# Kernel optimization log

Hardware: AMD Instinct MI355X
Metric: run time of the kernel (lower is better)

The kernel has to match this reference:

```python
import jax, jax.numpy as jnp
import numpy as np

DIM = 512
NUM_HEADS = 8
HEAD_DIM = DIM // NUM_HEADS
SCALE = HEAD_DIM ** -0.5


def setup_inputs() -> dict:
    key = jax.random.key(0)
    k1, k2, k3, k4 = jax.random.split(key, 4)
    x = jax.random.normal(k1, (4, 2048, DIM), dtype=jnp.float32)
    W_qkv = jax.random.normal(k2, (DIM, 3 * DIM), dtype=jnp.float32) * (DIM ** -0.5)
    W_proj = jax.random.normal(k3, (DIM, DIM), dtype=jnp.float32) * (DIM ** -0.5)
    b_proj = jax.random.normal(k4, (DIM,), dtype=jnp.float32) * 0.01
    return {"x": x, "W_qkv": W_qkv, "W_proj": W_proj, "b_proj": b_proj}


def reference(x, W_qkv, W_proj, b_proj):
    B, N, C = x.shape
    H, hd = NUM_HEADS, HEAD_DIM
    # qkv: [B, N, 3, H, hd] -> (q, k, v) each [B, H, N, hd]
    qkv = (x @ W_qkv).reshape(B, N, 3, H, hd)
    qkv = jnp.transpose(qkv, (2, 0, 3, 1, 4))
    q, k, v = qkv[0], qkv[1], qkv[2]
    # eager attention: [B, H, N, N]
    attn = jnp.einsum('bhnd,bhmd->bhnm', q, k) * SCALE
    attn = jax.nn.softmax(attn, axis=-1)
    out = jnp.einsum('bhnm,bhmd->bhnd', attn, v)  # [B, H, N, hd]
    out = jnp.transpose(out, (0, 2, 1, 3)).reshape(B, N, C)
    out = out @ W_proj + b_proj
    return (out, k, v)
```

## Files before the change

kernel.cpp:

```cpp
#include <hip/hip_runtime.h>

typedef unsigned short ushort_t;
typedef __bf16 bf16x8 __attribute__((ext_vector_type(8)));
typedef ushort_t u16x8 __attribute__((ext_vector_type(8)));
typedef float f32x4 __attribute__((ext_vector_type(4)));

#define MFMA(a, b, c) __builtin_amdgcn_mfma_f32_16x16x32_bf16(a, b, c, 0, 0, 0)

#define N_X      4194304L
#define N_WQKV   786432L
#define N_WPROJ  262144L
#define OUT_OFF_K 4194304L
#define OUT_OFF_V 8388608L

#define OFF_FLAG   0UL
#define OFF_XB     1024UL
#define OFF_WQKVT  (OFF_XB + 8388608UL)
#define OFF_WPROJT (OFF_WQKVT + 1572864UL)
#define OFF_BPROJ  (OFF_WPROJT + 524288UL)
#define OFF_QB     (OFF_BPROJ + 2048UL)
#define OFF_KB     (OFF_QB + 8388608UL)
#define OFF_VTB    (OFF_KB + 8388608UL)
#define OFF_ATTN   (OFF_VTB + 8388608UL)

#define QSCALE 0.180336880519191f

__device__ __forceinline__ ushort_t f2b(float f) {
    union { float f; unsigned u; } v; v.f = f;
    return (ushort_t)((v.u + 0x7FFFu + ((v.u >> 16) & 1u)) >> 16);
}
__device__ __forceinline__ float b2f(ushort_t h) {
    union { unsigned u; float f; } v; v.u = ((unsigned)h) << 16;
    return v.f;
}

__device__ __forceinline__ float fast_exp2(float x) {
#if __has_builtin(__builtin_amdgcn_exp2f)
    return __builtin_amdgcn_exp2f(x);
#else
    return __expf(x * 0.6931471805599453f);
#endif
}

__device__ __forceinline__ void glds16(const void* g, const void* l) {
    __builtin_amdgcn_global_load_lds((__attribute__((address_space(1))) void*)g,
                                     (__attribute__((address_space(3))) void*)l,
                                     16, 0, 0);
}

__device__ __forceinline__ int detect_bf16(const unsigned* __restrict__ x) {
    int lane = threadIdx.x & 63;
    int cnt = 0;
#pragma unroll
    for (int i = 0; i < 4; ++i) {
        unsigned w = x[lane + i * 64];
        float v = __uint_as_float((w & 0xFFFFu) << 16);
        float a = fabsf(v);
        if (a > 1e-3f && a < 100.0f) cnt++;
    }
#pragma unroll
    for (int off = 1; off < 64; off <<= 1) cnt += __shfl_xor(cnt, off, 64);
    return cnt > 128;
}

__global__ void k_prep(const void* __restrict__ xv, const void* __restrict__ wqv,
                       const void* __restrict__ wpv, const void* __restrict__ bpv,
                       ushort_t* __restrict__ xb, ushort_t* __restrict__ wqT,
                       ushort_t* __restrict__ wpT, float* __restrict__ bpf) {
    const int isb = detect_bf16((const unsigned*)xv);
    long i0 = (long)blockIdx.x * blockDim.x + threadIdx.x;
    long stride = (long)gridDim.x * blockDim.x;
    if (isb) {
        const ushort_t* x = (const ushort_t*)xv;
        const ushort_t* wq = (const ushort_t*)wqv;
        const ushort_t* wp = (const ushort_t*)wpv;
        const ushort_t* bp = (const ushort_t*)bpv;
        for (long i = i0; i < N_X / 8; i += stride)
            ((u16x8*)xb)[i] = ((const u16x8*)x)[i];
        for (long i = i0; i < N_WQKV / 8; i += stride) {
            long n = (i * 8) >> 9, k = (i * 8) & 511;
            u16x8 o;
#pragma unroll
            for (int e = 0; e < 8; ++e) o[e] = wq[(k + e) * 1536 + n];
            ((u16x8*)wqT)[i] = o;
        }
        for (long i = i0; i < N_WPROJ / 8; i += stride) {
            long n = (i * 8) >> 9, k = (i * 8) & 511;
            u16x8 o;
#pragma unroll
            for (int e = 0; e < 8; ++e) o[e] = wp[(k + e) * 512 + n];
            ((u16x8*)wpT)[i] = o;
        }
        for (long i = i0; i < 512; i += stride) bpf[i] = b2f(bp[i]);
    } else {
        const float* x = (const float*)xv;
        const float* wq = (const float*)wqv;
        const float* wp = (const float*)wpv;
        const float* bp = (const float*)bpv;
        for (long i = i0; i < N_X / 8; i += stride) {
            f32x4 a = ((const f32x4*)x)[i * 2], b = ((const f32x4*)x)[i * 2 + 1];
            u16x8 o;
#pragma unroll
            for (int e = 0; e < 4; ++e) { o[e] = f2b(a[e]); o[e + 4] = f2b(b[e]); }
            ((u16x8*)xb)[i] = o;
        }
        for (long i = i0; i < N_WQKV / 8; i += stride) {
            long n = (i * 8) >> 9, k = (i * 8) & 511;
            u16x8 o;
#pragma unroll
            for (int e = 0; e < 8; ++e) o[e] = f2b(wq[(k + e) * 1536 + n]);
            ((u16x8*)wqT)[i] = o;
        }
        for (long i = i0; i < N_WPROJ / 8; i += stride) {
            long n = (i * 8) >> 9, k = (i * 8) & 511;
            u16x8 o;
#pragma unroll
            for (int e = 0; e < 8; ++e) o[e] = f2b(wp[(k + e) * 512 + n]);
            ((u16x8*)wpT)[i] = o;
        }
        for (long i = i0; i < 512; i += stride) bpf[i] = bp[i];
    }
}

__global__ __launch_bounds__(256, 2)
void k_qkv(const unsigned* __restrict__ xraw,
           const ushort_t* __restrict__ xb, const ushort_t* __restrict__ wqT,
           ushort_t* __restrict__ qb, ushort_t* __restrict__ kb, ushort_t* __restrict__ vb,
           void* __restrict__ dout) {
    const int isb = detect_bf16(xraw);
    __shared__ __align__(16) ushort_t As[128 * 32];
    __shared__ __align__(16) ushort_t Bs[128 * 32];
    const int tid = threadIdx.x, wave = tid >> 6, lane = tid & 63;
    const int id = blockIdx.x;
    const int xcd = id & 7, g = id >> 3;
    const int bx = xcd * 8 + (g & 7);
    const int by = g >> 3;
    const int tm = bx * 128, tn = by * 128;
    const int wm = (wave >> 1) * 64, wn = (wave & 1) * 64;
    const int l15 = lane & 15, lq = lane >> 4;
    const int srow = lane >> 2, sc = lane & 3;

    f32x4 acc[4][4];
#pragma unroll
    for (int a = 0; a < 4; ++a)
#pragma unroll
        for (int b = 0; b < 4; ++b) acc[a][b] = (f32x4){0.f, 0.f, 0.f, 0.f};

    for (int k0 = 0; k0 < 512; k0 += 32) {
#pragma unroll
        for (int t = 0; t < 2; ++t) {
            int s = wave * 2 + t;
            int row = s * 16 + srow;
            int c = (sc ^ (row >> 1)) & 3;
            glds16(xb  + (long)(tm + row) * 512 + k0 + c * 8, As + s * 512);
            glds16(wqT + (long)(tn + row) * 512 + k0 + c * 8, Bs + s * 512);
        }
        __syncthreads();
        bf16x8 af[4], bfr[4];
#pragma unroll
        for (int mt = 0; mt < 4; ++mt) {
            int row = wm + mt * 16 + l15;
            int cp = (lq ^ (row >> 1)) & 3;
            af[mt] = *(const bf16x8*)(As + row * 32 + cp * 8);
        }
#pragma unroll
        for (int nt = 0; nt < 4; ++nt) {
            int row = wn + nt * 16 + l15;
            int cp = (lq ^ (row >> 1)) & 3;
            bfr[nt] = *(const bf16x8*)(Bs + row * 32 + cp * 8);
        }
#pragma unroll
        for (int mt = 0; mt < 4; ++mt)
#pragma unroll
            for (int nt = 0; nt < 4; ++nt)
                acc[mt][nt] = MFMA(af[mt], bfr[nt], acc[mt][nt]);
        __syncthreads();
    }

    float*    koutf = (float*)dout + OUT_OFF_K;
    float*    voutf = (float*)dout + OUT_OFF_V;
    ushort_t* koutb = (ushort_t*)dout + OUT_OFF_K;
    ushort_t* voutb = (ushort_t*)dout + OUT_OFF_V;
#pragma unroll
    for (int mt = 0; mt < 4; ++mt) {
#pragma unroll
        for (int nt = 0; nt < 4; ++nt) {
            int j = tn + wn + nt * 16 + l15;
            int t = j >> 9, h = (j >> 6) & 7, d = j & 63;
#pragma unroll
            for (int r = 0; r < 4; ++r) {
                int mm = tm + wm + mt * 16 + lq * 4 + r;
                int b = mm >> 11, nn = mm & 2047;
                float v = acc[mt][nt][r];
                long idx = ((long)(b * 8 + h) * 2048 + nn) * 64 + d;
                if (t == 0) {
                    qb[idx] = f2b(v * QSCALE);
                } else if (t == 1) {
                    kb[idx] = f2b(v);
                    if (isb) koutb[idx] = f2b(v); else koutf[idx] = v;
                } else {
                    vb[idx] = f2b(v);
                    if (isb) voutb[idx] = f2b(v); else voutf[idx] = v;
                }
            }
        }
    }
}

__global__ __launch_bounds__(256, 4)
void k_vtrans(const ushort_t* __restrict__ vb, ushort_t* __restrict__ vtb) {
    __shared__ ushort_t T[64 * 64];
    const int tid = threadIdx.x;
    const int bh = blockIdx.y, ktile = blockIdx.x;
    const long base = (long)bh * 131072 + (long)ktile * 64 * 64;
    const int row = tid >> 2, cq = tid & 3;
#pragma unroll
    for (int half = 0; half < 2; ++half) {
        int c = cq + half * 4;
        u16x8 v = *(const u16x8*)(vb + base + row * 64 + c * 8);
#pragma unroll
        for (int e = 0; e < 8; ++e) {
            int dim = c * 8 + e;
            T[row * 64 + ((dim + row) & 63)] = v[e];
        }
    }
    __syncthreads();
#pragma unroll
    for (int it = 0; it < 16; ++it) {
        int d = (tid >> 6) * 16 + it;
        int key = tid & 63;
        vtb[(long)bh * 131072 + (long)d * 2048 + ktile * 64 + key] =
            T[key * 64 + ((d + key) & 63)];
    }
}

__global__ __launch_bounds__(256, 2)
void k_attn(const ushort_t* __restrict__ qb, const ushort_t* __restrict__ kb,
            const ushort_t* __restrict__ vtb, ushort_t* __restrict__ attnb) {
    __shared__ __align__(16) ushort_t Kt[2][128 * 64];
    __shared__ __align__(16) ushort_t Vt[2][64 * 128];
    const int tid = threadIdx.x, wave = tid >> 6, lane = tid & 63;
    const int l15 = lane & 15, lq = lane >> 4;
    const int id = blockIdx.x;
    const int xcd = id & 7, g = id >> 3;
    const int bh = xcd * 4 + (g >> 4);
    const int qt = g & 15;
    const long kvbase = (long)bh * 131072;
    const long qbase = kvbase + (long)qt * 128 * 64;

    const int ksrow = lane >> 3, kschunk = lane & 7;
    const int vsrow = lane >> 4, vschunk = lane & 15;

    auto stage = [&](int j, int buf) {
#pragma unroll
        for (int t = 0; t < 4; ++t) {
            int s = wave * 4 + t;
            {
                int p = s * 8 + ksrow;
                int pos = p & 15;
                int akey = ((p >> 5) << 5) + ((pos >> 2) << 3) + (pos & 3) + ((p >> 4) & 1) * 4;
                int c = kschunk ^ (p & 7);
                glds16(kb + kvbase + (long)(j * 128 + akey) * 64 + c * 8, &Kt[buf][s * 512]);
            }
            {
                int row = s * 4 + vsrow;
                int c = vschunk ^ (row & 15);
                glds16(vtb + kvbase + (long)row * 2048 + j * 128 + c * 8, &Vt[buf][s * 512]);
            }
        }
    };

    stage(0, 0);

    bf16x8 aQ[2][2];
#pragma unroll
    for (int mq = 0; mq < 2; ++mq)
#pragma unroll
        for (int kt = 0; kt < 2; ++kt)
            aQ[mq][kt] = *(const bf16x8*)(qb + qbase +
                (long)(wave * 32 + mq * 16 + l15) * 64 + kt * 32 + lq * 8);

    union { ushort_t u[8]; bf16x8 v; } oneu;
#pragma unroll
    for (int i = 0; i < 8; ++i) oneu.u[i] = 0x3F80;
    const bf16x8 ones8 = oneu.v;

    f32x4 oacc[2][4], sum_acc[2];
#pragma unroll
    for (int mq = 0; mq < 2; ++mq) {
#pragma unroll
        for (int nd = 0; nd < 4; ++nd) oacc[mq][nd] = (f32x4){0.f, 0.f, 0.f, 0.f};
        sum_acc[mq] = (f32x4){0.f, 0.f, 0.f, 0.f};
    }

    for (int j = 0; j < 16; ++j) {
        int cur = j & 1;
        if (j < 15) {
            stage(j + 1, cur ^ 1);
            asm volatile("s_waitcnt vmcnt(8)" ::: "memory");
        } else {
            asm volatile("s_waitcnt vmcnt(0)" ::: "memory");
        }
        __builtin_amdgcn_sched_barrier(0);
        __builtin_amdgcn_s_barrier();

        const ushort_t* Ktc = &Kt[cur][0];
        const ushort_t* Vtc = &Vt[cur][0];

        f32x4 sacc[2][8];
#pragma unroll
        for (int mq = 0; mq < 2; ++mq)
#pragma unroll
            for (int nt = 0; nt < 8; ++nt) sacc[mq][nt] = (f32x4){0.f, 0.f, 0.f, 0.f};
#pragma unroll
        for (int nt = 0; nt < 8; ++nt) {
            int krow = nt * 16 + l15;
#pragma unroll
            for (int kt = 0; kt < 2; ++kt) {
                int c = (kt * 4 + lq) ^ (krow & 7);
                bf16x8 bk = *(const bf16x8*)(Ktc + krow * 64 + c * 8);
                sacc[0][nt] = MFMA(bk, aQ[0][kt], sacc[0][nt]);
                sacc[1][nt] = MFMA(bk, aQ[1][kt], sacc[1][nt]);
            }
        }

        bf16x8 pb8[2][4];
#pragma unroll
        for (int mq = 0; mq < 2; ++mq)
#pragma unroll
            for (int nt = 0; nt < 8; ++nt)
#pragma unroll
                for (int r = 0; r < 4; ++r)
                    pb8[mq][nt >> 1][(nt & 1) * 4 + r] =
                        (__bf16)fast_exp2(sacc[mq][nt][r]);

#pragma unroll
        for (int t = 0; t < 4; ++t) {
            sum_acc[0] = MFMA(ones8, pb8[0][t], sum_acc[0]);
            sum_acc[1] = MFMA(ones8, pb8[1][t], sum_acc[1]);
#pragma unroll
            for (int nd = 0; nd < 4; ++nd) {
                int drow = nd * 16 + l15;
                int cc = (t * 4 + lq) ^ (drow & 15);
                bf16x8 va = *(const bf16x8*)(Vtc + drow * 128 + cc * 8);
                oacc[0][nd] = MFMA(va, pb8[0][t], oacc[0][nd]);
                oacc[1][nd] = MFMA(va, pb8[1][t], oacc[1][nd]);
            }
        }

        asm volatile("s_waitcnt lgkmcnt(0)" ::: "memory");
        __builtin_amdgcn_sched_barrier(0);
        __builtin_amdgcn_s_barrier();
    }

    const int b = bh >> 3, hh = bh & 7;
#pragma unroll
    for (int mq = 0; mq < 2; ++mq) {
        float inv = 1.0f / sum_acc[mq][0];
        int n = qt * 128 + wave * 32 + mq * 16 + l15;
        long rowbase = ((long)b * 2048 + n) * 512 + hh * 64;
#pragma unroll
        for (int nd = 0; nd < 4; ++nd) {
            int d0 = nd * 16 + lq * 4;
            union { ushort_t u[4]; unsigned long long ll; } o;
#pragma unroll
            for (int r = 0; r < 4; ++r) o.u[r] = f2b(oacc[mq][nd][r] * inv);
            *(unsigned long long*)(attnb + rowbase + d0) = o.ll;
        }
    }
}

__global__ __launch_bounds__(256, 2)
void k_proj(const unsigned* __restrict__ xraw,
            const ushort_t* __restrict__ ab, const ushort_t* __restrict__ wpT,
            const float* __restrict__ bpf, void* __restrict__ dout) {
    const int isb = detect_bf16(xraw);
    __shared__ __align__(16) ushort_t As[128 * 32];
    __shared__ __align__(16) ushort_t Bs[128 * 32];
    const int tid = threadIdx.x, wave = tid >> 6, lane = tid & 63;
    const int id = blockIdx.x;
    const int xcd = id & 7, g = id >> 3;
    const int bx = xcd * 8 + (g & 7);
    const int by = g >> 3;
    const int tm = bx * 128, tn = by * 128;
    const int wm = (wave >> 1) * 64, wn = (wave & 1) * 64;
    const int l15 = lane & 15, lq = lane >> 4;
    const int srow = lane >> 2, sc = lane & 3;

    f32x4 acc[4][4];
#pragma unroll
    for (int a = 0; a < 4; ++a)
#pragma unroll
        for (int b = 0; b < 4; ++b) acc[a][b] = (f32x4){0.f, 0.f, 0.f, 0.f};

    for (int k0 = 0; k0 < 512; k0 += 32) {
#pragma unroll
        for (int t = 0; t < 2; ++t) {
            int s = wave * 2 + t;
            int row = s * 16 + srow;
            int c = (sc ^ (row >> 1)) & 3;
            glds16(ab  + (long)(tm + row) * 512 + k0 + c * 8, As + s * 512);
            glds16(wpT + (long)(tn + row) * 512 + k0 + c * 8, Bs + s * 512);
        }
        __syncthreads();
        bf16x8 af[4], bfr[4];
#pragma unroll
        for (int mt = 0; mt < 4; ++mt) {
            int row = wm + mt * 16 + l15;
            int cp = (lq ^ (row >> 1)) & 3;
            af[mt] = *(const bf16x8*)(As + row * 32 + cp * 8);
        }
#pragma unroll
        for (int nt = 0; nt < 4; ++nt) {
            int row = wn + nt * 16 + l15;
            int cp = (lq ^ (row >> 1)) & 3;
            bfr[nt] = *(const bf16x8*)(Bs + row * 32 + cp * 8);
        }
#pragma unroll
        for (int mt = 0; mt < 4; ++mt)
#pragma unroll
            for (int nt = 0; nt < 4; ++nt)
                acc[mt][nt] = MFMA(af[mt], bfr[nt], acc[mt][nt]);
        __syncthreads();
    }

#pragma unroll
    for (int mt = 0; mt < 4; ++mt) {
#pragma unroll
        for (int nt = 0; nt < 4; ++nt) {
            int j = tn + wn + nt * 16 + l15;
            float bias = bpf[j];
#pragma unroll
            for (int r = 0; r < 4; ++r) {
                int mm = tm + wm + mt * 16 + lq * 4 + r;
                float v = acc[mt][nt][r] + bias;
                if (isb) ((ushort_t*)dout)[(long)mm * 512 + j] = f2b(v);
                else     ((float*)dout)[(long)mm * 512 + j] = v;
            }
        }
    }
}

extern "C" void kernel_launch(void* const* d_in, const int* in_sizes, int n_in,
                              void* d_out, int out_size, void* d_ws, size_t ws_size,
                              hipStream_t stream) {
    (void)in_sizes; (void)n_in; (void)out_size; (void)ws_size;
    char* ws = (char*)d_ws;
    ushort_t* xb  = (ushort_t*)(ws + OFF_XB);
    ushort_t* wqT = (ushort_t*)(ws + OFF_WQKVT);
    ushort_t* wpT = (ushort_t*)(ws + OFF_WPROJT);
    float*    bpf = (float*)(ws + OFF_BPROJ);
    ushort_t* qb  = (ushort_t*)(ws + OFF_QB);
    ushort_t* kb  = (ushort_t*)(ws + OFF_KB);
    ushort_t* vtb = (ushort_t*)(ws + OFF_VTB);
    ushort_t* ab  = (ushort_t*)(ws + OFF_ATTN);
    ushort_t* vb  = (ushort_t*)(ws + OFF_ATTN);

    k_prep<<<1024, 256, 0, stream>>>(d_in[0], d_in[1], d_in[2], d_in[3],
                                     xb, wqT, wpT, bpf);

    k_qkv<<<768, 256, 0, stream>>>((const unsigned*)d_in[0], xb, wqT,
                                   qb, kb, vb, d_out);

    k_vtrans<<<dim3(32, 32), 256, 0, stream>>>(vb, vtb);

    k_attn<<<512, 256, 0, stream>>>(qb, kb, vtb, ab);

    k_proj<<<256, 256, 0, stream>>>((const unsigned*)d_in[0], ab, wpT, bpf, d_out);
}
```

Before: 167.2 us.

## Fuse V transpose into QKV epilogue and tile weight transposes via LDS

```diff
diff --git a/kernel.cpp b/kernel.cpp
--- a/kernel.cpp
+++ b/kernel.cpp
@@ -8,12 +8,9 @@
 #define MFMA(a, b, c) __builtin_amdgcn_mfma_f32_16x16x32_bf16(a, b, c, 0, 0, 0)
 
 #define N_X      4194304L
-#define N_WQKV   786432L
-#define N_WPROJ  262144L
 #define OUT_OFF_K 4194304L
 #define OUT_OFF_V 8388608L
 
-#define OFF_FLAG   0UL
 #define OFF_XB     1024UL
 #define OFF_WQKVT  (OFF_XB + 8388608UL)
 #define OFF_WPROJT (OFF_WQKVT + 1572864UL)
@@ -63,69 +60,81 @@
     return cnt > 128;
 }
 
-__global__ void k_prep(const void* __restrict__ xv, const void* __restrict__ wqv,
-                       const void* __restrict__ wpv, const void* __restrict__ bpv,
-                       ushort_t* __restrict__ xb, ushort_t* __restrict__ wqT,
-                       ushort_t* __restrict__ wpT, float* __restrict__ bpf) {
+__global__ __launch_bounds__(256)
+void k_prep(const void* __restrict__ xv, const void* __restrict__ wqv,
+            const void* __restrict__ wpv, const void* __restrict__ bpv,
+            ushort_t* __restrict__ xb, ushort_t* __restrict__ wqT,
+            ushort_t* __restrict__ wpT, float* __restrict__ bpf) {
     const int isb = detect_bf16((const unsigned*)xv);
-    long i0 = (long)blockIdx.x * blockDim.x + threadIdx.x;
-    long stride = (long)gridDim.x * blockDim.x;
-    if (isb) {
-        const ushort_t* x = (const ushort_t*)xv;
-        const ushort_t* wq = (const ushort_t*)wqv;
-        const ushort_t* wp = (const ushort_t*)wpv;
-        const ushort_t* bp = (const ushort_t*)bpv;
-        for (long i = i0; i < N_X / 8; i += stride)
-            ((u16x8*)xb)[i] = ((const u16x8*)x)[i];
-        for (long i = i0; i < N_WQKV / 8; i += stride) {
-            long n = (i * 8) >> 9, k = (i * 8) & 511;
-            u16x8 o;
-#pragma unroll
-            for (int e = 0; e < 8; ++e) o[e] = wq[(k + e) * 1536 + n];
-            ((u16x8*)wqT)[i] = o;
-        }
-        for (long i = i0; i < N_WPROJ / 8; i += stride) {
-            long n = (i * 8) >> 9, k = (i * 8) & 511;
-            u16x8 o;
-#pragma unroll
-            for (int e = 0; e < 8; ++e) o[e] = wp[(k + e) * 512 + n];
-            ((u16x8*)wpT)[i] = o;
-        }
-        for (long i = i0; i < 512; i += stride) bpf[i] = b2f(bp[i]);
+    const int bid = blockIdx.x, tid = threadIdx.x;
+    if (bid < 256) {
+        __shared__ ushort_t T[64 * 64];
+        int t = bid;
+        const void* src; ushort_t* dst; int ncols, tr, tc;
+        if (t < 192) { tr = t / 24; tc = t % 24; src = wqv; dst = wqT; ncols = 1536; }
+        else { t -= 192; tr = t >> 3; tc = t & 7; src = wpv; dst = wpT; ncols = 512; }
+        const int k0 = tr * 64, n0 = tc * 64;
+        const int row = tid >> 2, cq = tid & 3;
+        if (isb) {
+            const ushort_t* s = (const ushort_t*)src;
+#pragma unroll
+            for (int half = 0; half < 2; ++half) {
+                int c = cq + half * 4;
+                u16x8 v = *(const u16x8*)(s + (long)(k0 + row) * ncols + n0 + c * 8);
+#pragma unroll
+                for (int e = 0; e < 8; ++e) {
+                    int nl = c * 8 + e;
+                    T[row * 64 + ((nl + row) & 63)] = v[e];
+                }
+            }
+        } else {
+            const float* s = (const float*)src;
+#pragma unroll
+            for (int half = 0; half < 2; ++half) {
+                int c = cq + half * 4;
+                f32x4 a = *(const f32x4*)(s + (long)(k0 + row) * ncols + n0 + c * 8);
+                f32x4 b = *(const f32x4*)(s + (long)(k0 + row) * ncols + n0 + c * 8 + 4);
+#pragma unroll
+                for (int e = 0; e < 4; ++e) {
+                    T[row * 64 + ((c * 8 + e + row) & 63)] = f2b(a[e]);
+                    T[row * 64 + ((c * 8 + 4 + e + row) & 63)] = f2b(b[e]);
+                }
+            }
+        }
+        __syncthreads();
+#pragma unroll
+        for (int it = 0; it < 16; ++it) {
+            int nrow = (tid >> 6) * 16 + it;
+            int kcol = tid & 63;
+            dst[(long)(n0 + nrow) * 512 + k0 + kcol] = T[kcol * 64 + ((nrow + kcol) & 63)];
+        }
     } else {
-        const float* x = (const float*)xv;
-        const float* wq = (const float*)wqv;
-        const float* wp = (const float*)wpv;
-        const float* bp = (const float*)bpv;
-        for (long i = i0; i < N_X / 8; i += stride) {
-            f32x4 a = ((const f32x4*)x)[i * 2], b = ((const f32x4*)x)[i * 2 + 1];
-            u16x8 o;
-#pragma unroll
-            for (int e = 0; e < 4; ++e) { o[e] = f2b(a[e]); o[e + 4] = f2b(b[e]); }
-            ((u16x8*)xb)[i] = o;
-        }
-        for (long i = i0; i < N_WQKV / 8; i += stride) {
-            long n = (i * 8) >> 9, k = (i * 8) & 511;
-            u16x8 o;
-#pragma unroll
-            for (int e = 0; e < 8; ++e) o[e] = f2b(wq[(k + e) * 1536 + n]);
-            ((u16x8*)wqT)[i] = o;
-        }
-        for (long i = i0; i < N_WPROJ / 8; i += stride) {
-            long n = (i * 8) >> 9, k = (i * 8) & 511;
-            u16x8 o;
-#pragma unroll
-            for (int e = 0; e < 8; ++e) o[e] = f2b(wp[(k + e) * 512 + n]);
-            ((u16x8*)wpT)[i] = o;
-        }
-        for (long i = i0; i < 512; i += stride) bpf[i] = bp[i];
-    }
-}
-
-__global__ __launch_bounds__(256, 2)
+        long i0 = (long)(bid - 256) * 256 + tid;
+        long stride = (long)(gridDim.x - 256) * 256;
+        if (isb) {
+            const u16x8* x = (const u16x8*)xv;
+            for (long i = i0; i < N_X / 8; i += stride) ((u16x8*)xb)[i] = x[i];
+            const ushort_t* bp = (const ushort_t*)bpv;
+            for (long i = i0; i < 512; i += stride) bpf[i] = b2f(bp[i]);
+        } else {
+            const f32x4* x = (const f32x4*)xv;
+            for (long i = i0; i < N_X / 8; i += stride) {
+                f32x4 a = x[i * 2], b = x[i * 2 + 1];
+                u16x8 o;
+#pragma unroll
+                for (int e = 0; e < 4; ++e) { o[e] = f2b(a[e]); o[e + 4] = f2b(b[e]); }
+                ((u16x8*)xb)[i] = o;
+            }
+            const float* bp = (const float*)bpv;
+            for (long i = i0; i < 512; i += stride) bpf[i] = bp[i];
+        }
+    }
+}
+
+__global__ __launch_bounds__(256, 3)
 void k_qkv(const unsigned* __restrict__ xraw,
            const ushort_t* __restrict__ xb, const ushort_t* __restrict__ wqT,
-           ushort_t* __restrict__ qb, ushort_t* __restrict__ kb, ushort_t* __restrict__ vb,
+           ushort_t* __restrict__ qb, ushort_t* __restrict__ kb, ushort_t* __restrict__ vtb,
            void* __restrict__ dout) {
     const int isb = detect_bf16(xraw);
     __shared__ __align__(16) ushort_t As[128 * 32];
@@ -187,50 +196,33 @@
         for (int nt = 0; nt < 4; ++nt) {
             int j = tn + wn + nt * 16 + l15;
             int t = j >> 9, h = (j >> 6) & 7, d = j & 63;
-#pragma unroll
-            for (int r = 0; r < 4; ++r) {
-                int mm = tm + wm + mt * 16 + lq * 4 + r;
-                int b = mm >> 11, nn = mm & 2047;
-                float v = acc[mt][nt][r];
-                long idx = ((long)(b * 8 + h) * 2048 + nn) * 64 + d;
-                if (t == 0) {
-                    qb[idx] = f2b(v * QSCALE);
-                } else if (t == 1) {
-                    kb[idx] = f2b(v);
-                    if (isb) koutb[idx] = f2b(v); else koutf[idx] = v;
-                } else {
-                    vb[idx] = f2b(v);
-                    if (isb) voutb[idx] = f2b(v); else voutf[idx] = v;
+            int mm0 = tm + wm + mt * 16 + lq * 4;
+            int b = mm0 >> 11, nn0 = mm0 & 2047;
+            long base = ((long)(b * 8 + h) * 2048 + nn0) * 64 + d;
+            if (t == 0) {
+#pragma unroll
+                for (int r = 0; r < 4; ++r)
+                    qb[base + (long)r * 64] = f2b(acc[mt][nt][r] * QSCALE);
+            } else if (t == 1) {
+#pragma unroll
+                for (int r = 0; r < 4; ++r) {
+                    float v = acc[mt][nt][r];
+                    kb[base + (long)r * 64] = f2b(v);
+                    if (isb) koutb[base + (long)r * 64] = f2b(v);
+                    else     koutf[base + (long)r * 64] = v;
                 }
-            }
-        }
-    }
-}
-
-__global__ __launch_bounds__(256, 4)
-void k_vtrans(const ushort_t* __restrict__ vb, ushort_t* __restrict__ vtb) {
-    __shared__ ushort_t T[64 * 64];
-    const int tid = threadIdx.x;
-    const int bh = blockIdx.y, ktile = blockIdx.x;
-    const long base = (long)bh * 131072 + (long)ktile * 64 * 64;
-    const int row = tid >> 2, cq = tid & 3;
-#pragma unroll
-    for (int half = 0; half < 2; ++half) {
-        int c = cq + half * 4;
-        u16x8 v = *(const u16x8*)(vb + base + row * 64 + c * 8);
-#pragma unroll
-        for (int e = 0; e < 8; ++e) {
-            int dim = c * 8 + e;
-            T[row * 64 + ((dim + row) & 63)] = v[e];
-        }
-    }
-    __syncthreads();
-#pragma unroll
-    for (int it = 0; it < 16; ++it) {
-        int d = (tid >> 6) * 16 + it;
-        int key = tid & 63;
-        vtb[(long)bh * 131072 + (long)d * 2048 + ktile * 64 + key] =
-            T[key * 64 + ((d + key) & 63)];
+            } else {
+                union { ushort_t u[4]; unsigned long long ll; } o;
+#pragma unroll
+                for (int r = 0; r < 4; ++r) {
+                    float v = acc[mt][nt][r];
+                    o.u[r] = f2b(v);
+                    if (isb) voutb[base + (long)r * 64] = f2b(v);
+                    else     voutf[base + (long)r * 64] = v;
+                }
+                *(unsigned long long*)(vtb + ((long)(b * 8 + h) * 64 + d) * 2048 + nn0) = o.ll;
+            }
+        }
     }
 }
 
@@ -454,15 +446,12 @@
     ushort_t* kb  = (ushort_t*)(ws + OFF_KB);
     ushort_t* vtb = (ushort_t*)(ws + OFF_VTB);
     ushort_t* ab  = (ushort_t*)(ws + OFF_ATTN);
-    ushort_t* vb  = (ushort_t*)(ws + OFF_ATTN);
-
-    k_prep<<<1024, 256, 0, stream>>>(d_in[0], d_in[1], d_in[2], d_in[3],
+
+    k_prep<<<1280, 256, 0, stream>>>(d_in[0], d_in[1], d_in[2], d_in[3],
                                      xb, wqT, wpT, bpf);
 
     k_qkv<<<768, 256, 0, stream>>>((const unsigned*)d_in[0], xb, wqT,
-                                   qb, kb, vb, d_out);
-
-    k_vtrans<<<dim3(32, 32), 256, 0, stream>>>(vb, vtb);
+                                   qb, kb, vtb, d_out);
 
     k_attn<<<512, 256, 0, stream>>>(qb, kb, vtb, ab);
 
```

Result: faster. 158.3 us (-5.3%).
